# Performance work log

Hardware: AMD Instinct MI355X
Metric: run time of the kernel (lower is better)

The kernel has to match this reference:

```python
import jax, jax.numpy as jnp
import numpy as np

NUM_HEADS = 16

def rotate_half(x):
    h = x.shape[-1] // 2
    return jnp.concatenate([-x[..., h:], x[..., :h]], axis=-1)

def setup_inputs() -> dict:
    key = jax.random.key(0)
    k1, k2, k3 = jax.random.split(key, 3)
    B, S, H = 2, 2048, 1024
    x = jax.random.normal(k1, (B, S, H), dtype=jnp.float32)
    W_qkv = jax.random.normal(k2, (3 * H, H), dtype=jnp.float32) * (1.0 / np.sqrt(H))
    W_proj = jax.random.normal(k3, (H, H), dtype=jnp.float32) * (1.0 / np.sqrt(H))
    return {"x": x, "W_qkv": W_qkv, "W_proj": W_proj}

def reference(x, W_qkv, W_proj):
    B, S, H = x.shape
    nH = NUM_HEADS
    hd = H // nH
    # QKV projection (bias=False): y = x @ W.T
    qkv = jnp.einsum('bsh,oh->bso', x, W_qkv)  # [B,S,3H]
    q, k, v = jnp.split(qkv, 3, axis=-1)
    def to_heads(t):
        return t.reshape(B, S, nH, hd).transpose(0, 2, 1, 3)  # [B,nH,S,hd]
    q, k, v = to_heads(q), to_heads(k), to_heads(v)
    # RoPE on first half of head_dim; freqs dim = hd//2
    half = hd // 2
    inv_freq = 1.0 / (10000.0 ** (jnp.arange(0, hd, 2, dtype=jnp.float32) / hd))  # [hd//2]
    t = jnp.arange(S, dtype=jnp.float32)
    freqs = t[:, None] * inv_freq[None, :]  # [S, hd//2]
    cos = jnp.cos(freqs)[None, None]  # [1,1,S,hd//2]
    sin = jnp.sin(freqs)[None, None]
    q_half, q_rest = q[..., :half], q[..., half:]
    k_half, k_rest = k[..., :half], k[..., half:]
    q_rot = q_half * cos + rotate_half(q_half) * sin
    k_rot = k_half * cos + rotate_half(k_half) * sin
    q = jnp.concatenate([q_rot, q_rest], axis=-1)
    k = jnp.concatenate([k_rot, k_rest], axis=-1)
    # scaled dot-product attention (no mask, dropout=0 / eval)
    scale = 1.0 / np.sqrt(hd)
    att = jnp.einsum('bhqd,bhkd->bhqk', q, k) * scale  # [B,nH,S,S]
    att = jax.nn.softmax(att, axis=-1)
    out = jnp.einsum('bhqk,bhkd->bhqd', att, v)  # [B,nH,S,hd]
    out = out.transpose(0, 2, 1, 3).reshape(B, S, H)
    return jnp.einsum('bsh,oh->bso', out, W_proj)
```

## Files before the change

### kernel.cpp

```cpp
#include <hip/hip_runtime.h>
#include <math.h>

#define SEQ  2048
#define NHD  16
#define HD   64
#define HDIM 1024

typedef short s16x8 __attribute__((ext_vector_type(8)));
typedef short s16x4 __attribute__((ext_vector_type(4)));
typedef float f32x4 __attribute__((ext_vector_type(4)));

typedef const __attribute__((address_space(1))) unsigned int* gp_t;
typedef __attribute__((address_space(3))) unsigned int* lp_t;

__device__ __forceinline__ void async16(const short* g, short* l) {
    __builtin_amdgcn_global_load_lds((gp_t)g, (lp_t)l, 16, 0, 0);
}

__device__ __forceinline__ short f2bf(float f) {
    unsigned int u = __float_as_uint(f);
    u += 0x7fff + ((u >> 16) & 1);
    return (short)(u >> 16);
}
__device__ __forceinline__ float bf2f(short s) {
    return __uint_as_float(((unsigned int)(unsigned short)s) << 16);
}

__global__ void detect_k(const unsigned short* __restrict__ x, int* __restrict__ flag) {
    int cnt = 0;
    #pragma unroll 4
    for (int j = 0; j < 32; ++j) {
        unsigned short h = x[threadIdx.x * 32 + j];
        int e = (h >> 7) & 0xFF;
        cnt += (e >= 100 && e <= 140) ? 1 : 0;
    }
    __shared__ int tot;
    if (threadIdx.x == 0) tot = 0;
    __syncthreads();
    atomicAdd(&tot, cnt);
    __syncthreads();
    if (threadIdx.x == 0) *flag = (tot > (8192 * 9) / 10) ? 1 : 0;
}

#define XG4  (4096 * 1024 / 4)
#define WQG4 (3072 * 1024 / 4)
#define WPG4 (1024 * 1024 / 4)
__global__ void cvt_all_k(const void* __restrict__ xr, const void* __restrict__ wqr,
                          const void* __restrict__ wpr, short* __restrict__ xo,
                          short* __restrict__ wqo, short* __restrict__ wpo,
                          const int* __restrict__ flag) {
    int i = blockIdx.x * 256 + threadIdx.x;
    const void* in; short* out; int j;
    if (i < XG4)             { in = xr;  out = xo;  j = i; }
    else if (i < XG4 + WQG4) { in = wqr; out = wqo; j = i - XG4; }
    else                     { in = wpr; out = wpo; j = i - XG4 - WQG4; }
    if (*flag) {
        ((s16x4*)out)[j] = ((const s16x4*)in)[j];
    } else {
        f32x4 v = ((const f32x4*)in)[j];
        s16x4 r;
        r[0] = f2bf(v[0]); r[1] = f2bf(v[1]);
        r[2] = f2bf(v[2]); r[3] = f2bf(v[3]);
        ((s16x4*)out)[j] = r;
    }
}

__global__ void rope_tab_k(float2* __restrict__ tab) {
    int i = blockIdx.x * 256 + threadIdx.x;
    if (i >= SEQ * 32) return;
    int s = i >> 5, d = i & 31;
    float invf = (float)pow(10000.0, -(double)d / 32.0);
    float af = (float)s * invf;
    double a = (double)af;
    tab[i] = make_float2((float)cos(a), (float)sin(a));
}

template<int MODE>
__global__ __launch_bounds__(256, 2)
void gemm_bt(const short* __restrict__ A, const short* __restrict__ B,
             short* __restrict__ q, short* __restrict__ kbuf, short* __restrict__ vt,
             float* __restrict__ C, const float2* __restrict__ tab,
             int K, int N) {
    __shared__ __align__(16) short As[128 * 32];
    __shared__ __align__(16) short Bs[128 * 32];
    const int tid  = threadIdx.x;
    const int w    = tid >> 6, lane = tid & 63;
    const int quad = lane >> 4, l16 = lane & 15;
    const int wm = (w >> 1) * 64, wn = (w & 1) * 64;
    const int rowA0 = blockIdx.y * 128;
    const int colB0 = blockIdx.x * 128;

    f32x4 acc[4][4] = {};

    for (int kb = 0; kb < K; kb += 32) {
        __syncthreads();
        #pragma unroll
        for (int i = 0; i < 2; ++i) {
            int cidx = i * 256 + w * 64 + lane;
            int row = cidx >> 2, sc = cidx & 3;
            int c = sc ^ (row & 3);
            async16(&A[(long)(rowA0 + row) * K + kb + c * 8],
                    &As[(i * 256 + w * 64) * 8]);
            async16(&B[(long)(colB0 + row) * K + kb + c * 8],
                    &Bs[(i * 256 + w * 64) * 8]);
        }
        __syncthreads();

        s16x8 af[4], bfr[4];
        const int slot = quad ^ (l16 & 3);
        #pragma unroll
        for (int mi = 0; mi < 4; ++mi)
            af[mi] = *(const s16x8*)&As[(wm + mi * 16 + l16) * 32 + slot * 8];
        #pragma unroll
        for (int ni = 0; ni < 4; ++ni)
            bfr[ni] = *(const s16x8*)&Bs[(wn + ni * 16 + l16) * 32 + slot * 8];
        #pragma unroll
        for (int mi = 0; mi < 4; ++mi)
            #pragma unroll
            for (int ni = 0; ni < 4; ++ni)
                acc[mi][ni] = __builtin_amdgcn_mfma_f32_16x16x32_bf16(
                    af[mi], bfr[ni], acc[mi][ni], 0, 0, 0);
    }

    const int cb = colB0 + wn;
    if (MODE == 1) {
        #pragma unroll
        for (int mi = 0; mi < 4; ++mi) {
            #pragma unroll
            for (int r = 0; r < 4; ++r) {
                int gm = rowA0 + wm + mi * 16 + quad * 4 + r;
                float* cp = C + (long)gm * N + cb + l16;
                #pragma unroll
                for (int ni = 0; ni < 4; ++ni)
                    cp[ni * 16] = acc[mi][ni][r];
            }
        }
        return;
    }
    const int sector = cb >> 10;
    const int head   = (cb & 1023) >> 6;
    if (sector < 2) {
        const float sc = (sector == 0) ? 0.125f : 1.0f;
        #pragma unroll
        for (int mi = 0; mi < 4; ++mi) {
            #pragma unroll
            for (int r = 0; r < 4; ++r) {
                int gm = rowA0 + wm + mi * 16 + quad * 4 + r;
                int b = gm >> 11, s = gm & 2047;
                float v0 = acc[mi][0][r], v1 = acc[mi][1][r];
                float v2 = acc[mi][2][r], v3 = acc[mi][3][r];
                float2 cs0 = tab[s * 32 + l16];
                float2 cs1 = tab[s * 32 + 16 + l16];
                float n0 = v0 * cs0.x - v1 * cs0.y;
                float n1 = v1 * cs1.x + v0 * cs1.y;
                short* dst = (sector == 0 ? q : kbuf)
                           + ((long)((b * NHD + head) * SEQ + s)) * HD + l16;
                dst[0]  = f2bf(n0 * sc);  dst[16] = f2bf(n1 * sc);
                dst[32] = f2bf(v2 * sc);  dst[48] = f2bf(v3 * sc);
            }
        }
    } else {
        #pragma unroll
        for (int mi = 0; mi < 4; ++mi) {
            int srow = rowA0 + wm + mi * 16 + quad * 4;
            int b = srow >> 11, s0 = srow & 2047;
            #pragma unroll
            for (int ni = 0; ni < 4; ++ni) {
                s16x4 pk;
                #pragma unroll
                for (int r = 0; r < 4; ++r) pk[r] = f2bf(acc[mi][ni][r]);
                *(s16x4*)&vt[((long)((b * NHD + head) * HD + ni * 16 + l16)) * SEQ + s0] = pk;
            }
        }
    }
}

__global__ __launch_bounds__(256, 2)
void flash_attn(const short* __restrict__ Q, const short* __restrict__ K,
                const short* __restrict__ Vt, short* __restrict__ opart,
                float2* __restrict__ mlpart) {
    __shared__ __align__(16) short Qs[128 * 64];
    __shared__ __align__(16) short Ks[64 * 64];
    __shared__ __align__(16) short Vs[64 * 64];
    const int tid  = threadIdx.x;
    const int w    = tid >> 6, lane = tid & 63;
    const int quad = lane >> 4, l16 = lane & 15;
    const int bh = blockIdx.y;
    const int qb = blockIdx.x * 128;
    const int z  = blockIdx.z;
    const short* Qp = Q  + (long)bh * SEQ * HD + (long)qb * HD;
    const short* Kp = K  + (long)bh * SEQ * HD;
    const short* Vp = Vt + (long)bh * HD * SEQ;

    #pragma unroll
    for (int i = 0; i < 4; ++i) {
        int cidx = i * 256 + w * 64 + lane;
        int row = cidx >> 3, sc = cidx & 7;
        int c = sc ^ (row & 7);
        async16(&Qp[row * HD + c * 8], &Qs[(i * 256 + w * 64) * 8]);
    }
    __syncthreads();
    s16x8 aq[2][2];
    #pragma unroll
    for (int mi = 0; mi < 2; ++mi)
        #pragma unroll
        for (int ks = 0; ks < 2; ++ks)
            aq[mi][ks] = *(const s16x8*)&Qs[(w * 32 + mi * 16 + l16) * 64
                                            + ((ks * 4 + quad) ^ (l16 & 7)) * 8];

    s16x8 ones8;
    #pragma unroll
    for (int j = 0; j < 8; ++j) ones8[j] = (short)0x3F80;

    float m_i[2] = {-1e30f, -1e30f};
    f32x4 oacc[2][4] = {};
    f32x4 lacc[2] = {};

    for (int kt = z * 16; kt < z * 16 + 16; ++kt) {
        __syncthreads();
        #pragma unroll
        for (int i = 0; i < 2; ++i) {
            int cidx = i * 256 + w * 64 + lane;
            int row = cidx >> 3, sc = cidx & 7;
            int c = sc ^ (row & 7);
            async16(&Kp[(kt * 64 + row) * HD + c * 8], &Ks[(i * 256 + w * 64) * 8]);
            async16(&Vp[(long)row * SEQ + kt * 64 + c * 8], &Vs[(i * 256 + w * 64) * 8]);
        }
        __syncthreads();

        f32x4 st[2][4] = {};
        #pragma unroll
        for (int ki = 0; ki < 4; ++ki) {
            s16x8 ak0 = *(const s16x8*)&Ks[(ki * 16 + l16) * 64 + (quad ^ (l16 & 7)) * 8];
            s16x8 ak1 = *(const s16x8*)&Ks[(ki * 16 + l16) * 64 + ((4 + quad) ^ (l16 & 7)) * 8];
            #pragma unroll
            for (int mi = 0; mi < 2; ++mi) {
                st[mi][ki] = __builtin_amdgcn_mfma_f32_16x16x32_bf16(
                    ak0, aq[mi][0], st[mi][ki], 0, 0, 0);
                st[mi][ki] = __builtin_amdgcn_mfma_f32_16x16x32_bf16(
                    ak1, aq[mi][1], st[mi][ki], 0, 0, 0);
            }
        }

        s16x8 bp[2][2];
        #pragma unroll
        for (int mi = 0; mi < 2; ++mi) {
            float mx = st[mi][0][0];
            #pragma unroll
            for (int ki = 0; ki < 4; ++ki)
                #pragma unroll
                for (int r = 0; r < 4; ++r) mx = fmaxf(mx, st[mi][ki][r]);
            mx = fmaxf(mx, __shfl_xor(mx, 16));
            mx = fmaxf(mx, __shfl_xor(mx, 32));
            float mn = fmaxf(m_i[mi], mx);
            float alpha = __expf(m_i[mi] - mn);
            m_i[mi] = mn;
            #pragma unroll
            for (int t = 0; t < 2; ++t) {
                s16x8 f;
                #pragma unroll
                for (int r = 0; r < 4; ++r) {
                    f[r]     = f2bf(__expf(st[mi][2 * t][r] - mn));
                    f[4 + r] = f2bf(__expf(st[mi][2 * t + 1][r] - mn));
                }
                bp[mi][t] = f;
            }
            #pragma unroll
            for (int nd = 0; nd < 4; ++nd) oacc[mi][nd] *= alpha;
            lacc[mi] *= alpha;
        }

        #pragma unroll
        for (int t = 0; t < 2; ++t) {
            #pragma unroll
            for (int nd = 0; nd < 4; ++nd) {
                int d = nd * 16 + l16;
                s16x4 va = *(const s16x4*)&Vs[d * 64
                             + ((4 * t + (quad >> 1)) ^ (l16 & 7)) * 8
                             + (quad & 1) * 4];
                s16x4 vb = *(const s16x4*)&Vs[d * 64
                             + ((4 * t + 2 + (quad >> 1)) ^ (l16 & 7)) * 8
                             + (quad & 1) * 4];
                s16x8 av = {va[0], va[1], va[2], va[3],
                            vb[0], vb[1], vb[2], vb[3]};
                #pragma unroll
                for (int mi = 0; mi < 2; ++mi)
                    oacc[mi][nd] = __builtin_amdgcn_mfma_f32_16x16x32_bf16(
                        av, bp[mi][t], oacc[mi][nd], 0, 0, 0);
            }
            #pragma unroll
            for (int mi = 0; mi < 2; ++mi)
                lacc[mi] = __builtin_amdgcn_mfma_f32_16x16x32_bf16(
                    ones8, bp[mi][t], lacc[mi], 0, 0, 0);
        }
    }

    #pragma unroll
    for (int mi = 0; mi < 2; ++mi) {
        int srow = qb + w * 32 + mi * 16 + l16;
        long prow = (long)(z * 32 + bh) * SEQ + srow;
        if (quad == 0) mlpart[prow] = make_float2(m_i[mi], lacc[mi][0]);
        short* op = opart + prow * 64 + quad * 4;
        #pragma unroll
        for (int nd = 0; nd < 4; ++nd) {
            s16x4 pk;
            #pragma unroll
            for (int r = 0; r < 4; ++r) pk[r] = f2bf(oacc[mi][nd][r]);
            *(s16x4*)&op[nd * 16] = pk;
        }
    }
}

__global__ __launch_bounds__(256)
void merge_k(const short* __restrict__ opart, const float2* __restrict__ mlpart,
             short* __restrict__ att) {
    int idx = blockIdx.x * 256 + threadIdx.x;
    int t16 = idx & 15, rowg = idx >> 4;
    int bh = rowg >> 11, srow = rowg & 2047;
    float2 ml1 = mlpart[rowg];
    float2 ml2 = mlpart[65536 + rowg];
    float m  = fmaxf(ml1.x, ml2.x);
    float w1 = __expf(ml1.x - m), w2 = __expf(ml2.x - m);
    float inv = 1.0f / (w1 * ml1.y + w2 * ml2.y);
    w1 *= inv; w2 *= inv;
    s16x4 o1 = *(const s16x4*)&opart[(long)rowg * 64 + t16 * 4];
    s16x4 o2 = *(const s16x4*)&opart[(long)(65536 + rowg) * 64 + t16 * 4];
    int b = bh >> 4, h = bh & 15;
    short* dst = att + ((long)(b * SEQ + srow)) * HDIM + h * HD + t16 * 4;
    s16x4 r;
    #pragma unroll
    for (int j = 0; j < 4; ++j)
        r[j] = f2bf(w1 * bf2f(o1[j]) + w2 * bf2f(o2[j]));
    *(s16x4*)dst = r;
}

extern "C" void kernel_launch(void* const* d_in, const int* in_sizes, int n_in,
                              void* d_out, int out_size, void* d_ws, size_t ws_size,
                              hipStream_t stream) {
    const void* x_raw  = d_in[0];
    const void* Wq_raw = d_in[1];
    const void* Wp_raw = d_in[2];
    for (int i = 0; i < n_in; ++i) {
        if      (in_sizes[i] == 4096 * 1024) x_raw  = d_in[i];
        else if (in_sizes[i] == 3072 * 1024) Wq_raw = d_in[i];
        else if (in_sizes[i] == 1024 * 1024) Wp_raw = d_in[i];
    }
    float* out = (float*)d_out;

    const size_t MB = 1u << 20;
    char* ws = (char*)d_ws;
    short*  q     = (short*)(ws);
    short*  k     = (short*)(ws +  8 * MB);
    short*  vt    = (short*)(ws + 16 * MB);
    short*  xbf   = (short*)(ws + 24 * MB);
    short*  att   = xbf;
    short*  wqkv  = (short*)(ws + 32 * MB);
    short*  wprj  = (short*)(ws + 38 * MB);
    float2* tab   = (float2*)(ws + 40 * MB);
    int*    flag  = (int*)(ws + 40 * MB + 512 * 1024);
    short*  opart = (short*)(ws + 41 * MB);
    float2* mlprt = (float2*)(ws + 57 * MB);

    detect_k<<<dim3(1), dim3(256), 0, stream>>>((const unsigned short*)x_raw, flag);

    cvt_all_k<<<dim3((XG4 + WQG4 + WPG4) / 256), dim3(256), 0, stream>>>(
        x_raw, Wq_raw, Wp_raw, xbf, wqkv, wprj, flag);

    rope_tab_k<<<dim3(SEQ * 32 / 256), dim3(256), 0, stream>>>(tab);

    gemm_bt<0><<<dim3(3072 / 128, 4096 / 128), dim3(256), 0, stream>>>(
        xbf, wqkv, q, k, vt, (float*)nullptr, tab, 1024, 3072);

    flash_attn<<<dim3(SEQ / 128, 2 * NHD, 2), dim3(256), 0, stream>>>(
        q, k, vt, opart, mlprt);

    merge_k<<<dim3(65536 * 16 / 256), dim3(256), 0, stream>>>(opart, mlprt, att);

    gemm_bt<1><<<dim3(1024 / 128, 4096 / 128), dim3(256), 0, stream>>>(
        att, wprj, (short*)nullptr, (short*)nullptr, (short*)nullptr, out, tab, 1024, 1024);
}
```

Baseline: 205.9 us.

## Stage QK epilogue through LDS, use exp2 softmax, allow 4-way KV split

The Q/K epilogue of the QKV GEMM now writes rotated tiles into shared memory and stores them to global as coalesced 16-byte rows instead of scattered 2-byte writes. The Q scale folds in log2(e) so the softmax can use exp2f. Flash attention drops the Q shared-memory stage and loads Q fragments straight from global, which frees LDS for 4 blocks per CU. The number of KV splits becomes a runtime parameter (4 when the workspace is large enough), with merge_k generalized to match. This adds parallelism and occupancy but costs more partial-output traffic and a heavier merge, and the new launch bound may cause register spills.

```diff
diff --git a/kernel.cpp b/kernel.cpp
--- a/kernel.cpp
+++ b/kernel.cpp
@@ -140,23 +140,40 @@
     const int sector = cb >> 10;
     const int head   = (cb & 1023) >> 6;
     if (sector < 2) {
-        const float sc = (sector == 0) ? 0.125f : 1.0f;
-        #pragma unroll
-        for (int mi = 0; mi < 4; ++mi) {
-            #pragma unroll
-            for (int r = 0; r < 4; ++r) {
-                int gm = rowA0 + wm + mi * 16 + quad * 4 + r;
-                int b = gm >> 11, s = gm & 2047;
-                float v0 = acc[mi][0][r], v1 = acc[mi][1][r];
-                float v2 = acc[mi][2][r], v3 = acc[mi][3][r];
-                float2 cs0 = tab[s * 32 + l16];
-                float2 cs1 = tab[s * 32 + 16 + l16];
-                float n0 = v0 * cs0.x - v1 * cs0.y;
-                float n1 = v1 * cs1.x + v0 * cs1.y;
-                short* dst = (sector == 0 ? q : kbuf)
-                           + ((long)((b * NHD + head) * SEQ + s)) * HD + l16;
-                dst[0]  = f2bf(n0 * sc);  dst[16] = f2bf(n1 * sc);
-                dst[32] = f2bf(v2 * sc);  dst[48] = f2bf(v3 * sc);
+        const float sc = (sector == 0) ? 0.18033688f : 1.0f;
+        __syncthreads();
+        short* arena = (w < 2) ? (As + w * 2048) : (Bs + (w - 2) * 2048);
+        const int gmb = rowA0 + wm;
+        const int b = gmb >> 11, s0 = gmb & 2047;
+        short* dst0 = (sector == 0 ? q : kbuf)
+                    + ((long)((b * NHD + head) * SEQ + s0)) * HD;
+        #pragma unroll
+        for (int hh = 0; hh < 2; ++hh) {
+            #pragma unroll
+            for (int m2 = 0; m2 < 2; ++m2) {
+                int mi = hh * 2 + m2;
+                #pragma unroll
+                for (int r = 0; r < 4; ++r) {
+                    int lrow = m2 * 16 + quad * 4 + r;
+                    int s = s0 + hh * 32 + lrow;
+                    float v0 = acc[mi][0][r], v1 = acc[mi][1][r];
+                    float v2 = acc[mi][2][r], v3 = acc[mi][3][r];
+                    float2 cs0 = tab[s * 32 + l16];
+                    float2 cs1 = tab[s * 32 + 16 + l16];
+                    float n0 = v0 * cs0.x - v1 * cs0.y;
+                    float n1 = v1 * cs1.x + v0 * cs1.y;
+                    arena[lrow * 64 + l16]      = f2bf(n0 * sc);
+                    arena[lrow * 64 + l16 + 16] = f2bf(n1 * sc);
+                    arena[lrow * 64 + l16 + 32] = f2bf(v2 * sc);
+                    arena[lrow * 64 + l16 + 48] = f2bf(v3 * sc);
+                }
+            }
+            #pragma unroll
+            for (int it = 0; it < 4; ++it) {
+                int chunk = it * 64 + lane;
+                int row = chunk >> 3, cc = chunk & 7;
+                s16x8 vv = *(const s16x8*)&arena[row * 64 + cc * 8];
+                *(s16x8*)&dst0[(hh * 32 + row) * HD + cc * 8] = vv;
             }
         }
     } else {
@@ -175,11 +192,10 @@
     }
 }
 
-__global__ __launch_bounds__(256, 2)
+__global__ __launch_bounds__(256, 4)
 void flash_attn(const short* __restrict__ Q, const short* __restrict__ K,
                 const short* __restrict__ Vt, short* __restrict__ opart,
-                float2* __restrict__ mlpart) {
-    __shared__ __align__(16) short Qs[128 * 64];
+                float2* __restrict__ mlpart, int nt) {
     __shared__ __align__(16) short Ks[64 * 64];
     __shared__ __align__(16) short Vs[64 * 64];
     const int tid  = threadIdx.x;
@@ -192,21 +208,13 @@
     const short* Kp = K  + (long)bh * SEQ * HD;
     const short* Vp = Vt + (long)bh * HD * SEQ;
 
-    #pragma unroll
-    for (int i = 0; i < 4; ++i) {
-        int cidx = i * 256 + w * 64 + lane;
-        int row = cidx >> 3, sc = cidx & 7;
-        int c = sc ^ (row & 7);
-        async16(&Qp[row * HD + c * 8], &Qs[(i * 256 + w * 64) * 8]);
-    }
-    __syncthreads();
     s16x8 aq[2][2];
     #pragma unroll
     for (int mi = 0; mi < 2; ++mi)
         #pragma unroll
         for (int ks = 0; ks < 2; ++ks)
-            aq[mi][ks] = *(const s16x8*)&Qs[(w * 32 + mi * 16 + l16) * 64
-                                            + ((ks * 4 + quad) ^ (l16 & 7)) * 8];
+            aq[mi][ks] = *(const s16x8*)&Qp[(w * 32 + mi * 16 + l16) * HD
+                                            + ks * 32 + quad * 8];
 
     s16x8 ones8;
     #pragma unroll
@@ -216,7 +224,7 @@
     f32x4 oacc[2][4] = {};
     f32x4 lacc[2] = {};
 
-    for (int kt = z * 16; kt < z * 16 + 16; ++kt) {
+    for (int kt = z * nt; kt < z * nt + nt; ++kt) {
         __syncthreads();
         #pragma unroll
         for (int i = 0; i < 2; ++i) {
@@ -253,15 +261,15 @@
             mx = fmaxf(mx, __shfl_xor(mx, 16));
             mx = fmaxf(mx, __shfl_xor(mx, 32));
             float mn = fmaxf(m_i[mi], mx);
-            float alpha = __expf(m_i[mi] - mn);
+            float alpha = exp2f(m_i[mi] - mn);
             m_i[mi] = mn;
             #pragma unroll
             for (int t = 0; t < 2; ++t) {
                 s16x8 f;
                 #pragma unroll
                 for (int r = 0; r < 4; ++r) {
-                    f[r]     = f2bf(__expf(st[mi][2 * t][r] - mn));
-                    f[4 + r] = f2bf(__expf(st[mi][2 * t + 1][r] - mn));
+                    f[r]     = f2bf(exp2f(st[mi][2 * t][r] - mn));
+                    f[4 + r] = f2bf(exp2f(st[mi][2 * t + 1][r] - mn));
                 }
                 bp[mi][t] = f;
             }
@@ -298,7 +306,7 @@
     #pragma unroll
     for (int mi = 0; mi < 2; ++mi) {
         int srow = qb + w * 32 + mi * 16 + l16;
-        long prow = (long)(z * 32 + bh) * SEQ + srow;
+        long prow = (long)(z * 2 * NHD + bh) * SEQ + srow;
         if (quad == 0) mlpart[prow] = make_float2(m_i[mi], lacc[mi][0]);
         short* op = opart + prow * 64 + quad * 4;
         #pragma unroll
@@ -313,24 +321,31 @@
 
 __global__ __launch_bounds__(256)
 void merge_k(const short* __restrict__ opart, const float2* __restrict__ mlpart,
-             short* __restrict__ att) {
+             short* __restrict__ att, int ns) {
     int idx = blockIdx.x * 256 + threadIdx.x;
     int t16 = idx & 15, rowg = idx >> 4;
     int bh = rowg >> 11, srow = rowg & 2047;
-    float2 ml1 = mlpart[rowg];
-    float2 ml2 = mlpart[65536 + rowg];
-    float m  = fmaxf(ml1.x, ml2.x);
-    float w1 = __expf(ml1.x - m), w2 = __expf(ml2.x - m);
-    float inv = 1.0f / (w1 * ml1.y + w2 * ml2.y);
-    w1 *= inv; w2 *= inv;
-    s16x4 o1 = *(const s16x4*)&opart[(long)rowg * 64 + t16 * 4];
-    s16x4 o2 = *(const s16x4*)&opart[(long)(65536 + rowg) * 64 + t16 * 4];
+    float m = -1e30f;
+    for (int z = 0; z < ns; ++z) m = fmaxf(m, mlpart[z * 65536 + rowg].x);
+    float wz[4];
+    float den = 0.f;
+    for (int z = 0; z < ns; ++z) {
+        float2 ml = mlpart[z * 65536 + rowg];
+        wz[z] = exp2f(ml.x - m);
+        den += wz[z] * ml.y;
+    }
+    float inv = 1.0f / den;
+    float o[4] = {0.f, 0.f, 0.f, 0.f};
+    for (int z = 0; z < ns; ++z) {
+        s16x4 ov = *(const s16x4*)&opart[((long)z * 65536 + rowg) * 64 + t16 * 4];
+        #pragma unroll
+        for (int j = 0; j < 4; ++j) o[j] += wz[z] * bf2f(ov[j]);
+    }
     int b = bh >> 4, h = bh & 15;
     short* dst = att + ((long)(b * SEQ + srow)) * HDIM + h * HD + t16 * 4;
     s16x4 r;
     #pragma unroll
-    for (int j = 0; j < 4; ++j)
-        r[j] = f2bf(w1 * bf2f(o1[j]) + w2 * bf2f(o2[j]));
+    for (int j = 0; j < 4; ++j) r[j] = f2bf(o[j] * inv);
     *(s16x4*)dst = r;
 }
 
@@ -358,8 +373,11 @@
     short*  wprj  = (short*)(ws + 38 * MB);
     float2* tab   = (float2*)(ws + 40 * MB);
     int*    flag  = (int*)(ws + 40 * MB + 512 * 1024);
+
+    const int ns = (ws_size >= 80 * MB) ? 4 : 2;
+    const int nt = 32 / ns;
     short*  opart = (short*)(ws + 41 * MB);
-    float2* mlprt = (float2*)(ws + 57 * MB);
+    float2* mlprt = (float2*)(ws + 41 * MB + (size_t)ns * 8 * MB);
 
     detect_k<<<dim3(1), dim3(256), 0, stream>>>((const unsigned short*)x_raw, flag);
 
@@ -371,10 +389,10 @@
     gemm_bt<0><<<dim3(3072 / 128, 4096 / 128), dim3(256), 0, stream>>>(
         xbf, wqkv, q, k, vt, (float*)nullptr, tab, 1024, 3072);
 
-    flash_attn<<<dim3(SEQ / 128, 2 * NHD, 2), dim3(256), 0, stream>>>(
-        q, k, vt, opart, mlprt);
-
-    merge_k<<<dim3(65536 * 16 / 256), dim3(256), 0, stream>>>(opart, mlprt, att);
+    flash_attn<<<dim3(SEQ / 128, 2 * NHD, ns), dim3(256), 0, stream>>>(
+        q, k, vt, opart, mlprt, nt);
+
+    merge_k<<<dim3(65536 * 16 / 256), dim3(256), 0, stream>>>(opart, mlprt, att, ns);
 
     gemm_bt<1><<<dim3(1024 / 128, 4096 / 128), dim3(256), 0, stream>>>(
         att, wprj, (short*)nullptr, (short*)nullptr, (short*)nullptr, out, tab, 1024, 1024);
```

After: 224.5 us. 9.0% more time.
